# Kernel tuning notes

Measured on AMD Instinct MI355X. Metric: run time of the kernel, lower is better.

## Reference

```python
import jax, jax.numpy as jnp
import numpy as np

N_NODES = 50000
N_EDGES = 600000
IN_F = 128
HID_F = 128
OUT_F = 128


def setup_inputs() -> dict:
    key = jax.random.key(0)
    ks = jax.random.split(key, 12)
    features = jax.random.normal(ks[0], (N_NODES, IN_F), dtype=jnp.float32)
    src = jax.random.randint(ks[1], (N_EDGES,), 0, N_NODES, dtype=jnp.int32)
    dst = jax.random.randint(ks[2], (N_EDGES,), 0, N_NODES, dtype=jnp.int32)

    def lin(k, fan_in, fan_out):
        s = 1.0 / jnp.sqrt(fan_in)
        return jax.random.uniform(k, (fan_in, fan_out), jnp.float32, -s, s)

    return {
        "features": features, "src": src, "dst": dst,
        "W1_self": lin(ks[3], IN_F, HID_F), "W1_neigh": lin(ks[4], IN_F, HID_F),
        "b1": jnp.zeros((HID_F,), jnp.float32),
        "W2_self": lin(ks[5], HID_F, HID_F), "W2_neigh": lin(ks[6], HID_F, HID_F),
        "b2": jnp.zeros((HID_F,), jnp.float32),
        "W3_self": lin(ks[7], HID_F, OUT_F), "W3_neigh": lin(ks[8], HID_F, OUT_F),
        "b3": jnp.zeros((OUT_F,), jnp.float32),
    }


def _sage_mean(x, src, dst, W_self, W_neigh, b):
    # gather source-node features along edges, mean-reduce into dst nodes
    msgs = x[src]                                                # [E, d]
    summed = jax.ops.segment_sum(msgs, dst, num_segments=N_NODES)  # [N, d]
    deg = jax.ops.segment_sum(jnp.ones((dst.shape[0],), x.dtype), dst,
                              num_segments=N_NODES)               # [N]
    mean = summed / jnp.maximum(deg, 1.0)[:, None]
    return x @ W_self + mean @ W_neigh + b


def reference(features, src, dst,
              W1_self, W1_neigh, b1,
              W2_self, W2_neigh, b2,
              W3_self, W3_neigh, b3):
    x = features.reshape(features.shape[0], -1)  # Flatten (no-op for 2D)
    x = jax.nn.relu(_sage_mean(x, src, dst, W1_self, W1_neigh, b1))
    x = jax.nn.relu(_sage_mean(x, src, dst, W2_self, W2_neigh, b2))
    x = _sage_mean(x, src, dst, W3_self, W3_neigh, b3)
    return x
```

## Files before the change

kernel.cpp:

```cpp
#include <hip/hip_runtime.h>

#define NN 50000
#define NE 600000
#define F 128

typedef __attribute__((ext_vector_type(4))) float f4;
typedef __attribute__((ext_vector_type(4))) float f32x4;
typedef __bf16 bf16x8 __attribute__((ext_vector_type(8)));
typedef short short8v __attribute__((ext_vector_type(8)));
typedef unsigned short u16x8 __attribute__((ext_vector_type(8)));

__device__ inline ushort f2bf(float f) {
    uint u = __builtin_bit_cast(uint, f);
    uint r = (u + 0x7FFFu + ((u >> 16) & 1u)) >> 16;
    return (ushort)r;
}
__device__ inline float bf2f(ushort u) {
    uint t = ((uint)u) << 16;
    return __builtin_bit_cast(float, t);
}


__global__ void count_deg(const int* __restrict__ dst, int* __restrict__ deg, int E) {
    int e = blockIdx.x * blockDim.x + threadIdx.x;
    if (e < E) atomicAdd(&deg[dst[e]], 1);
}

__global__ __launch_bounds__(1024) void scan_part1(const int* __restrict__ deg,
                                                   int* __restrict__ bsum, int N) {
    __shared__ int ws[16];
    int tid = threadIdx.x;
    int idx = blockIdx.x * 1024 + tid;
    int v = (idx < N) ? deg[idx] : 0;
    #pragma unroll
    for (int o = 32; o; o >>= 1) v += __shfl_down(v, o);
    if ((tid & 63) == 0) ws[tid >> 6] = v;
    __syncthreads();
    if (tid < 64) {
        int t = (tid < 16) ? ws[tid] : 0;
        #pragma unroll
        for (int o = 8; o; o >>= 1) t += __shfl_down(t, o);
        if (tid == 0) bsum[blockIdx.x] = t;
    }
}

__global__ __launch_bounds__(1024) void scan_part3(const int* __restrict__ deg,
                                                   const int* __restrict__ bsum,
                                                   int* __restrict__ off,
                                                   int* __restrict__ cur,
                                                   float* __restrict__ recip,
                                                   int N, int NB) {
    __shared__ int wsum[16];
    __shared__ int sbase;
    int tid = threadIdx.x;
    int wid = tid >> 6;
    int lane = tid & 63;
    if (tid < 64) {
        int v = (tid < NB) ? bsum[tid] : 0;
        int x = v;
        #pragma unroll
        for (int o = 1; o < 64; o <<= 1) {
            int t = __shfl_up(x, o);
            if (lane >= o) x += t;
        }
        if (tid == blockIdx.x) sbase = x - v;
    }
    int idx = blockIdx.x * 1024 + tid;
    int v = (idx < N) ? deg[idx] : 0;
    int x = v;
    #pragma unroll
    for (int o = 1; o < 64; o <<= 1) {
        int t = __shfl_up(x, o);
        if (lane >= o) x += t;
    }
    if (lane == 63) wsum[wid] = x;
    __syncthreads();
    if (tid == 0) {
        int a = 0;
        #pragma unroll
        for (int w = 0; w < 16; ++w) { int t = wsum[w]; wsum[w] = a; a += t; }
    }
    __syncthreads();
    int incl = x + wsum[wid];
    if (idx < N) {
        int start = sbase + incl - v;
        off[idx] = start;
        cur[idx] = start;
        recip[idx] = 1.0f / (float)max(v, 1);
    }
}

__global__ void fill_csr(const int* __restrict__ src, const int* __restrict__ dst,
                         int* __restrict__ cur, int* __restrict__ csr, int E) {
    int e = blockIdx.x * blockDim.x + threadIdx.x;
    if (e < E) {
        int pos = atomicAdd(&cur[dst[e]], 1);
        csr[pos] = src[e];
    }
}


__global__ __launch_bounds__(256) void wt_prep(const float* __restrict__ W1s, const float* __restrict__ W1n,
                                               const float* __restrict__ W2s, const float* __restrict__ W2n,
                                               const float* __restrict__ W3s, const float* __restrict__ W3n,
                                               ushort* __restrict__ Bt1, ushort* __restrict__ Bt2,
                                               ushort* __restrict__ Bt3) {
    int layer = blockIdx.y;
    const float* Ws = (layer == 0) ? W1s : (layer == 1) ? W2s : W3s;
    const float* Wn = (layer == 0) ? W1n : (layer == 1) ? W2n : W3n;
    ushort* Bt = (layer == 0) ? Bt1 : (layer == 1) ? Bt2 : Bt3;
    int col = blockIdx.x;
    int k = threadIdx.x;
    float v = (k < 128) ? Ws[k * 128 + col] : Wn[(k - 128) * 128 + col];
    Bt[col * 256 + k] = f2bf(v);
}


__global__ __launch_bounds__(256) void to_bf16(const float* __restrict__ in,
                                               ushort* __restrict__ out, int n8) {
    int i = blockIdx.x * 256 + threadIdx.x;
    if (i < n8) {
        const f4* p = (const f4*)in + (size_t)i * 2;
        f4 a = p[0], b = p[1];
        short8v w;
        w[0] = (short)f2bf(a[0]); w[1] = (short)f2bf(a[1]);
        w[2] = (short)f2bf(a[2]); w[3] = (short)f2bf(a[3]);
        w[4] = (short)f2bf(b[0]); w[5] = (short)f2bf(b[1]);
        w[6] = (short)f2bf(b[2]); w[7] = (short)f2bf(b[3]);
        ((short8v*)out)[i] = w;
    }
}


template <int RELU, int OUTBF>
__global__ __launch_bounds__(256) void sage_layer(const ushort* __restrict__ xb,
                                                  const int* __restrict__ off,
                                                  const int* __restrict__ deg,
                                                  const float* __restrict__ recip,
                                                  const int* __restrict__ csr,
                                                  const ushort* __restrict__ Bt,
                                                  const float* __restrict__ bias,
                                                  void* __restrict__ outp, int N) {
    __shared__ ushort sa[32 * 256];
    __shared__ int wcnt;
    int tid = threadIdx.x;
    int r0 = blockIdx.x * 32;
    if (tid == 0) wcnt = 0;

    {
        int row = tid >> 3;
        int c = tid & 7;
        int grow = r0 + row;
        uint sw = ((uint)row & 7u) << 4;
        uint base = (uint)(row * 512 + c * 32);
        short8v w0 = (short8v)0, w1 = (short8v)0;
        if (grow < N) {
            const short8v* sp = (const short8v*)&xb[(size_t)grow * 128 + c * 16];
            w0 = sp[0]; w1 = sp[1];
        }
        *(short8v*)((char*)sa + (base ^ sw)) = w0;
        *(short8v*)((char*)sa + ((base + 16) ^ sw)) = w1;
    }
    __syncthreads();

    {
        int l16 = tid & 15;
        int lanebase = (tid & 63) & ~15;
        const ushort* xpb = xb + (size_t)l16 * 8;
        for (;;) {
            int n = 0;
            if (l16 == 0) n = atomicAdd(&wcnt, 1);
            n = __shfl(n, lanebase);
            if (n >= 32) break;
            int row = n;
            int node = r0 + row;
            float a[8] = {0.f, 0.f, 0.f, 0.f, 0.f, 0.f, 0.f, 0.f};
            if (node < N) {
                int start = off[node];
                int d = deg[node];
                int dm1 = (d > 0) ? d - 1 : 0;
                for (int i = 0; i < d; i += 16) {
                    int rem = d - i;
                    int s[16];
                    #pragma unroll
                    for (int u = 0; u < 16; ++u) {
                        int idx = i + u;
                        s[u] = csr[start + ((idx < dm1) ? idx : dm1)];
                    }
                    u16x8 v[16];
                    #pragma unroll
                    for (int u = 0; u < 16; ++u) v[u] = *(const u16x8*)(xpb + (size_t)s[u] * 128);
                    #pragma unroll
                    for (int u = 0; u < 16; ++u) {
                        float m = (u < rem) ? 1.f : 0.f;
                        #pragma unroll
                        for (int j = 0; j < 8; ++j) a[j] += m * bf2f(v[u][j]);
                    }
                }
                float r = recip[node];
                #pragma unroll
                for (int j = 0; j < 8; ++j) a[j] *= r;
            }
            short8v w;
            #pragma unroll
            for (int j = 0; j < 8; ++j) w[j] = (short)f2bf(a[j]);
            uint sw = ((uint)row & 7u) << 4;
            uint addr = (uint)(row * 512 + 256 + l16 * 16);
            *(short8v*)((char*)sa + (addr ^ sw)) = w;
        }
    }
    __syncthreads();

    int lane = tid & 63;
    int wid = tid >> 6;
    int wr = wid & 1;
    int wc = wid >> 1;
    int l15 = lane & 15;
    int lg = lane >> 4;

    int arow = wr * 16 + l15;
    uint abase = (uint)(arow * 512 + lg * 16);
    uint asw = ((uint)arow & 7u) << 4;
    bf16x8 a[8];
    #pragma unroll
    for (int ks = 0; ks < 8; ++ks) {
        a[ks] = *(const bf16x8*)((const char*)sa + ((abase + (uint)ks * 64) ^ asw));
    }

    f32x4 acc[4];
    #pragma unroll
    for (int ct = 0; ct < 4; ++ct) acc[ct] = (f32x4)0.f;

    #pragma unroll
    for (int ct = 0; ct < 4; ++ct) {
        int bcol = wc * 64 + ct * 16 + l15;
        const ushort* bp = Bt + bcol * 256 + lg * 8;
        #pragma unroll
        for (int ks = 0; ks < 8; ++ks) {
            bf16x8 b = *(const bf16x8*)(bp + ks * 32);
            acc[ct] = __builtin_amdgcn_mfma_f32_16x16x32_bf16(a[ks], b, acc[ct], 0, 0, 0);
        }
    }

    int crow = r0 + wr * 16 + lg * 4;
    #pragma unroll
    for (int ct = 0; ct < 4; ++ct) {
        int col = wc * 64 + ct * 16 + l15;
        float bv = bias[col];
        #pragma unroll
        for (int r = 0; r < 4; ++r) {
            int row = crow + r;
            if (row < N) {
                float v = acc[ct][r] + bv;
                if (RELU) v = fmaxf(v, 0.f);
                if (OUTBF) ((ushort*)outp)[(size_t)row * 128 + col] = f2bf(v);
                else       ((float*)outp)[(size_t)row * 128 + col] = v;
            }
        }
    }
}


extern "C" void kernel_launch(void* const* d_in, const int* in_sizes, int n_in,
                              void* d_out, int out_size, void* d_ws, size_t ws_size,
                              hipStream_t stream) {
    const float* feat = (const float*)d_in[0];
    const int* src = (const int*)d_in[1];
    const int* dst = (const int*)d_in[2];
    const float* W1s = (const float*)d_in[3];
    const float* W1n = (const float*)d_in[4];
    const float* b1 = (const float*)d_in[5];
    const float* W2s = (const float*)d_in[6];
    const float* W2n = (const float*)d_in[7];
    const float* b2 = (const float*)d_in[8];
    const float* W3s = (const float*)d_in[9];
    const float* W3n = (const float*)d_in[10];
    const float* b3 = (const float*)d_in[11];
    float* out = (float*)d_out;

    const int N = NN, E = NE;
    const int NB = (N + 1023) / 1024;

    char* p = (char*)d_ws;
    auto alloc = [&](size_t bytes) {
        char* q = p;
        p += (bytes + 255) & ~(size_t)255;
        return q;
    };
    int* deg = (int*)alloc((size_t)N * 4);
    int* off = (int*)alloc((size_t)N * 4);
    int* cur = (int*)alloc((size_t)N * 4);
    float* recip = (float*)alloc((size_t)N * 4);
    int* bsum = (int*)alloc(64 * 4);
    int* csr = (int*)alloc((size_t)E * 4);
    ushort* xb0 = (ushort*)alloc((size_t)N * F * 2);
    ushort* h1b = (ushort*)alloc((size_t)N * F * 2);
    ushort* h2b = (ushort*)alloc((size_t)N * F * 2);
    ushort* Bt1 = (ushort*)alloc(128 * 256 * 2);
    ushort* Bt2 = (ushort*)alloc(128 * 256 * 2);
    ushort* Bt3 = (ushort*)alloc(128 * 256 * 2);

    wt_prep<<<dim3(128, 3), 256, 0, stream>>>(W1s, W1n, W2s, W2n, W3s, W3n, Bt1, Bt2, Bt3);
    to_bf16<<<(N * F / 8 + 255) / 256, 256, 0, stream>>>(feat, xb0, N * F / 8);

    hipMemsetAsync(deg, 0, (size_t)N * 4, stream);
    count_deg<<<(E + 255) / 256, 256, 0, stream>>>(dst, deg, E);
    scan_part1<<<NB, 1024, 0, stream>>>(deg, bsum, N);
    scan_part3<<<NB, 1024, 0, stream>>>(deg, bsum, off, cur, recip, N, NB);
    fill_csr<<<(E + 255) / 256, 256, 0, stream>>>(src, dst, cur, csr, E);

    int grid = (N + 31) / 32;

    sage_layer<1, 1><<<grid, 256, 0, stream>>>(xb0, off, deg, recip, csr, Bt1, b1, h1b, N);
    sage_layer<1, 1><<<grid, 256, 0, stream>>>(h1b, off, deg, recip, csr, Bt2, b2, h2b, N);
    sage_layer<0, 0><<<grid, 256, 0, stream>>>(h2b, off, deg, recip, csr, Bt3, b3, out, N);
}
```

Before: 275.1 us.

## Replace atomic work-stealing aggregation with static row-per-thread feature-chunk mapping

```diff
diff --git a/kernel.cpp b/kernel.cpp
--- a/kernel.cpp
+++ b/kernel.cpp
@@ -142,10 +142,8 @@
                                                   const float* __restrict__ bias,
                                                   void* __restrict__ outp, int N) {
     __shared__ ushort sa[32 * 256];
-    __shared__ int wcnt;
     int tid = threadIdx.x;
     int r0 = blockIdx.x * 32;
-    if (tid == 0) wcnt = 0;
 
     {
         int row = tid >> 3;
@@ -161,53 +159,57 @@
         *(short8v*)((char*)sa + (base ^ sw)) = w0;
         *(short8v*)((char*)sa + ((base + 16) ^ sw)) = w1;
     }
-    __syncthreads();
 
     {
-        int l16 = tid & 15;
-        int lanebase = (tid & 63) & ~15;
-        const ushort* xpb = xb + (size_t)l16 * 8;
-        for (;;) {
-            int n = 0;
-            if (l16 == 0) n = atomicAdd(&wcnt, 1);
-            n = __shfl(n, lanebase);
-            if (n >= 32) break;
-            int row = n;
-            int node = r0 + row;
-            float a[8] = {0.f, 0.f, 0.f, 0.f, 0.f, 0.f, 0.f, 0.f};
-            if (node < N) {
-                int start = off[node];
-                int d = deg[node];
-                int dm1 = (d > 0) ? d - 1 : 0;
-                for (int i = 0; i < d; i += 16) {
-                    int rem = d - i;
-                    int s[16];
+        int row = tid & 31;
+        int ch = tid >> 5;
+        int node = r0 + row;
+        const ushort* xpb = xb + (size_t)ch * 16;
+        float a[16];
+        #pragma unroll
+        for (int j = 0; j < 16; ++j) a[j] = 0.f;
+        if (node < N) {
+            int start = off[node];
+            int d = deg[node];
+            int dm1 = (d > 0) ? d - 1 : 0;
+            for (int i = 0; i < d; i += 4) {
+                int s[4];
+                #pragma unroll
+                for (int u = 0; u < 4; ++u) {
+                    int idx = i + u;
+                    s[u] = csr[start + ((idx < dm1) ? idx : dm1)];
+                }
+                u16x8 v0[4], v1[4];
+                #pragma unroll
+                for (int u = 0; u < 4; ++u) {
+                    const ushort* rp = xpb + (size_t)s[u] * 128;
+                    v0[u] = *(const u16x8*)rp;
+                    v1[u] = *(const u16x8*)(rp + 8);
+                }
+                #pragma unroll
+                for (int u = 0; u < 4; ++u) {
+                    float m = (i + u < d) ? 1.f : 0.f;
                     #pragma unroll
-                    for (int u = 0; u < 16; ++u) {
-                        int idx = i + u;
-                        s[u] = csr[start + ((idx < dm1) ? idx : dm1)];
-                    }
-                    u16x8 v[16];
-                    #pragma unroll
-                    for (int u = 0; u < 16; ++u) v[u] = *(const u16x8*)(xpb + (size_t)s[u] * 128);
-                    #pragma unroll
-                    for (int u = 0; u < 16; ++u) {
-                        float m = (u < rem) ? 1.f : 0.f;
-                        #pragma unroll
-                        for (int j = 0; j < 8; ++j) a[j] += m * bf2f(v[u][j]);
+                    for (int j = 0; j < 8; ++j) {
+                        a[j] += m * bf2f(v0[u][j]);
+                        a[8 + j] += m * bf2f(v1[u][j]);
                     }
                 }
-                float r = recip[node];
-                #pragma unroll
-                for (int j = 0; j < 8; ++j) a[j] *= r;
             }
-            short8v w;
+            float r = recip[node];
             #pragma unroll
-            for (int j = 0; j < 8; ++j) w[j] = (short)f2bf(a[j]);
-            uint sw = ((uint)row & 7u) << 4;
-            uint addr = (uint)(row * 512 + 256 + l16 * 16);
-            *(short8v*)((char*)sa + (addr ^ sw)) = w;
-        }
+            for (int j = 0; j < 16; ++j) a[j] *= r;
+        }
+        short8v w0, w1;
+        #pragma unroll
+        for (int j = 0; j < 8; ++j) {
+            w0[j] = (short)f2bf(a[j]);
+            w1[j] = (short)f2bf(a[8 + j]);
+        }
+        uint sw = ((uint)row & 7u) << 4;
+        uint addr = (uint)(row * 512 + 256 + ch * 32);
+        *(short8v*)((char*)sa + (addr ^ sw)) = w0;
+        *(short8v*)((char*)sa + ((addr + 16) ^ sw)) = w1;
     }
     __syncthreads();
 
```

Measured after the change: 270.4 us. No clear change (-1.7%).
